# Performance work log

Measured on AMD Instinct MI355X. Metric: run time of the kernel, lower is better.

Reference implementation:

```python
import jax, jax.numpy as jnp
import numpy as np

NEG = -9e9  # large negative used by the original torch code for masking


def setup_inputs() -> dict:
    key = jax.random.key(0)
    k1, k2, k3, k4 = jax.random.split(key, 4)
    B, N, L, D = 64, 128, 64, 768
    return {
        "text_embeddings": jax.random.normal(k1, (B, N, D), dtype=jnp.float32),
        "image_embeddings": jax.random.normal(k2, (B, L, D), dtype=jnp.float32),
        "text_mask": jax.random.randint(k3, (B, N), 0, 2, dtype=jnp.int32),
        "image_mask": jax.random.randint(k4, (B, L), 0, 2, dtype=jnp.int32),
    }


def _grounding(text_emb, image_emb, text_mask, image_mask):
    # Vectorized version of the B x B python loop in score_grounding.
    tm = text_mask.astype(text_emb.dtype)   # [B, N]
    im = image_mask.astype(text_emb.dtype)  # [B, L]
    # pairwise mask: mask[i, j, n, l] = text_mask[i, n] * image_mask[j, l]
    mask = tm[:, None, :, None] * im[None, :, None, :]            # [B, B, N, L]
    att = jnp.einsum('ind,jld->ijnl', text_emb, image_emb) * mask  # [B, B, N, L]
    att = jnp.where(att * mask != 0, att, NEG)
    # softmax over image spans (last dim), masked
    aw_first = jax.nn.softmax(att, axis=-1) * mask
    score1 = (aw_first * att).sum(-1).mean(-1)                     # [B, B]
    # softmax over text spans (dim 2 == the N axis), masked (transpose trick in torch)
    aw_second = jax.nn.softmax(att, axis=2) * mask
    score2 = (aw_second * att).sum(-1).mean(-1)                    # [B, B]
    sent_scores = score1 + score2                                  # [B, B]
    B = text_emb.shape[0]
    idx = jnp.arange(B)
    token_scores = att[idx, idx]                                   # diagonal pairs, [B, N, L]
    return sent_scores, token_scores


def reference(text_embeddings, image_embeddings, text_mask, image_mask):
    B = text_embeddings.shape[0]
    S, token_scores = _grounding(text_embeddings, image_embeddings, text_mask, image_mask)
    # text_emb_i2s = softmax(att_weights) @ image_emb
    text_emb_i2s = jnp.einsum('bnl,bld->bnd', jax.nn.softmax(token_scores, axis=-1), image_embeddings)
    # loss = -(sum diag logsoftmax(S, dim=1) + sum diag logsoftmax(S.T, dim=1)) / n
    ls1 = jnp.diagonal(jax.nn.log_softmax(S, axis=1))
    ls2 = jnp.diagonal(jax.nn.log_softmax(S.T, axis=1))
    loss = -(jnp.sum(ls1) + jnp.sum(ls2)) / B
    return loss, text_emb_i2s
```

## Files before the change

### kernel.cpp

```cpp
#include <hip/hip_runtime.h>
#include <math.h>

#define BSZ 64
#define NN  128
#define LL  64
#define DD  768
#define NEGV (-9e9f)

#define TQ (BSZ * NN * DD / 4)
#define IQ (BSZ * LL * DD / 4)

typedef _Float16 f16x8 __attribute__((ext_vector_type(8)));
typedef __attribute__((ext_vector_type(4))) float f32x4;

__device__ __forceinline__ void gl_lds16(const void* g, void* l) {
    __builtin_amdgcn_global_load_lds(
        (const __attribute__((address_space(1))) void*)g,
        (__attribute__((address_space(3))) void*)l, 16, 0, 0);
}

__global__ __launch_bounds__(256) void k_prep(
    const float4* __restrict__ t4, const float4* __restrict__ g4,
    ushort4* __restrict__ A, ushort4* __restrict__ B)
{
    int id = blockIdx.x * 256 + threadIdx.x;
    const float4* src; ushort4* dst; int idx;
    if (id < TQ) { src = t4; dst = A; idx = id; }
    else         { src = g4; dst = B; idx = id - TQ; }
    float4 x = src[idx];
    _Float16 h0 = (_Float16)x.x, h1 = (_Float16)x.y;
    _Float16 h2 = (_Float16)x.z, h3 = (_Float16)x.w;
    ushort4 o;
    o.x = __builtin_bit_cast(unsigned short, h0);
    o.y = __builtin_bit_cast(unsigned short, h1);
    o.z = __builtin_bit_cast(unsigned short, h2);
    o.w = __builtin_bit_cast(unsigned short, h3);
    dst[idx] = o;
}

__device__ __forceinline__ void stage_chunk(
    const unsigned short* __restrict__ pa, const unsigned short* __restrict__ pb,
    int k0, char* buf, int wave, int lane)
{
    int rsub = lane >> 3;
    int k8s  = lane & 7;
#pragma unroll
    for (int c = 0; c < 4; c++) {
        int r  = c * 64 + wave * 8 + rsub;
        int k8 = k8s ^ (r & 7);
        gl_lds16(pa + (size_t)r * DD + k0 + k8 * 8, buf + c * 8192 + wave * 1024);
        gl_lds16(pb + (size_t)r * DD + k0 + k8 * 8, buf + 32768 + c * 8192 + wave * 1024);
    }
}

__global__ __launch_bounds__(512, 2) void k_scores(
    const unsigned short* __restrict__ A, const unsigned short* __restrict__ B,
    const int* __restrict__ tmask, const int* __restrict__ imask,
    float* __restrict__ S, float* __restrict__ W)
{
    __shared__ __align__(16) char stage[2][65536];
    __shared__ float tmi[256];
    __shared__ float imj[256];
    __shared__ float rowredL[256][4];
    __shared__ float cpmax[4][256];
    __shared__ float cpes[4][256];
    __shared__ float cpws[4][256];

    const int bid = blockIdx.x;
    const int grp = bid >> 4, idx = bid & 15;
    const int ip = (grp >> 2) * 4 + (idx >> 2);
    const int jq = (grp & 3) * 4 + (idx & 3);

    const int tid  = threadIdx.x;
    const int wave = tid >> 6;
    const int lane = tid & 63;
    const int quad = lane >> 4;
    const int l15  = lane & 15;
    const int wr   = wave & 3;
    const int wc   = wave >> 2;
    const int ih   = wr >> 1;

    if (tid < 256) tmi[tid] = tmask[ip * 256 + tid] ? 1.f : 0.f;
    else           imj[tid - 256] = imask[jq * 256 + (tid - 256)] ? 1.f : 0.f;

    const unsigned short* pa = A + (size_t)ip * 2 * NN * DD;
    const unsigned short* pb = B + (size_t)jq * 4 * LL * DD;

    f32x4 acc[4][8];
    const f32x4 zf = {0.f, 0.f, 0.f, 0.f};
#pragma unroll
    for (int tr = 0; tr < 4; tr++)
#pragma unroll
        for (int tc = 0; tc < 8; tc++) acc[tr][tc] = zf;

    stage_chunk(pa, pb, 0, stage[0], wave, lane);
    __syncthreads();

    for (int c = 0; c < 12; c++) {
        if (c + 1 < 12)
            stage_chunk(pa, pb, (c + 1) << 6, stage[(c + 1) & 1], wave, lane);
        const char* Ab = stage[c & 1];
        const char* Bb = Ab + 32768;
#pragma unroll
        for (int s = 0; s < 2; s++) {
            int sw = (((s * 4 + quad) ^ (l15 & 7)) << 4);
            f16x8 af[4], bfr[8];
#pragma unroll
            for (int tr = 0; tr < 4; tr++) {
                int row = wr * 64 + tr * 16 + l15;
                af[tr] = *(const f16x8*)(Ab + (row << 7) + sw);
            }
#pragma unroll
            for (int tc = 0; tc < 8; tc++) {
                int col = wc * 128 + tc * 16 + l15;
                bfr[tc] = *(const f16x8*)(Bb + (col << 7) + sw);
            }
#pragma unroll
            for (int tr = 0; tr < 4; tr++)
#pragma unroll
                for (int tc = 0; tc < 8; tc++)
                    acc[tr][tc] = __builtin_amdgcn_mfma_f32_16x16x32_f16(
                        af[tr], bfr[tc], acc[tr][tc], 0, 0, 0);
        }
        __syncthreads();
    }

    float tmr[4][4];
    float imc[8];
#pragma unroll
    for (int tr = 0; tr < 4; tr++)
#pragma unroll
        for (int rr = 0; rr < 4; rr++)
            tmr[tr][rr] = tmi[wr * 64 + tr * 16 + quad * 4 + rr];
#pragma unroll
    for (int tc = 0; tc < 8; tc++)
        imc[tc] = imj[wc * 128 + tc * 16 + l15];

    const bool isdiag = (jq == (ip >> 1));
    const int  jneed  = ip * 2 + ih - jq * 4;

#pragma unroll
    for (int tr = 0; tr < 4; tr++) {
#pragma unroll
        for (int rr = 0; rr < 4; rr++) {
            int row = wr * 64 + tr * 16 + quad * 4 + rr;
            float tm = tmr[tr][rr];
#pragma unroll
            for (int jl = 0; jl < 2; jl++) {
                float vmv[4];
                float m = -INFINITY;
#pragma unroll
                for (int t = 0; t < 4; t++) {
                    int tc = jl * 4 + t;
                    float v = acc[tr][tc][rr];
                    float vm = (tm != 0.f && imc[tc] != 0.f && v != 0.f) ? v : NEGV;
                    vmv[t] = vm;
                    m = fmaxf(m, vm);
                }
                m = fmaxf(m, __shfl_xor(m, 1));
                m = fmaxf(m, __shfl_xor(m, 2));
                m = fmaxf(m, __shfl_xor(m, 4));
                m = fmaxf(m, __shfl_xor(m, 8));
                float ss = 0.f, ws = 0.f;
#pragma unroll
                for (int t = 0; t < 4; t++) {
                    float e = __expf(vmv[t] - m);
                    ss += e;
                    ws += imc[jl * 4 + t] * e * vmv[t];
                }
                ss += __shfl_xor(ss, 1); ss += __shfl_xor(ss, 2);
                ss += __shfl_xor(ss, 4); ss += __shfl_xor(ss, 8);
                ws += __shfl_xor(ws, 1); ws += __shfl_xor(ws, 2);
                ws += __shfl_xor(ws, 4); ws += __shfl_xor(ws, 8);
                if (l15 == 0) rowredL[row][wc * 2 + jl] = tm * (ws / ss);
                if (isdiag && (wc * 2 + jl) == jneed) {
                    float inv = 1.f / ss;
                    float* Wb = W + (size_t)(ip * 2 + ih) * LL * NN;
                    int n = row & 127;
#pragma unroll
                    for (int t = 0; t < 4; t++) {
                        float e = __expf(vmv[t] - m) * inv;
                        Wb[(size_t)(t * 16 + l15) * NN + n] = e;
                    }
                }
            }
        }
    }

#pragma unroll
    for (int tc = 0; tc < 8; tc++) {
        int col = wc * 128 + tc * 16 + l15;
        float cm = -INFINITY;
#pragma unroll
        for (int tr = 0; tr < 4; tr++)
#pragma unroll
            for (int rr = 0; rr < 4; rr++) {
                float v = acc[tr][tc][rr];
                float vm = (tmr[tr][rr] != 0.f && imc[tc] != 0.f && v != 0.f) ? v : NEGV;
                cm = fmaxf(cm, vm);
            }
        cm = fmaxf(cm, __shfl_xor(cm, 16));
        cm = fmaxf(cm, __shfl_xor(cm, 32));
        if (quad == 0) cpmax[wr][col] = cm;
    }
    __syncthreads();

#pragma unroll
    for (int tc = 0; tc < 8; tc++) {
        int col = wc * 128 + tc * 16 + l15;
        float m2 = fmaxf(cpmax[ih * 2][col], cpmax[ih * 2 + 1][col]);
        float es = 0.f, ws = 0.f;
#pragma unroll
        for (int tr = 0; tr < 4; tr++)
#pragma unroll
            for (int rr = 0; rr < 4; rr++) {
                float v = acc[tr][tc][rr];
                float tm = tmr[tr][rr];
                float vm = (tm != 0.f && imc[tc] != 0.f && v != 0.f) ? v : NEGV;
                float e = __expf(vm - m2);
                es += e;
                ws += tm * e * vm;
            }
        es += __shfl_xor(es, 16); es += __shfl_xor(es, 32);
        ws += __shfl_xor(ws, 16); ws += __shfl_xor(ws, 32);
        if (quad == 0) { cpes[wr][col] = es; cpws[wr][col] = ws; }
    }
    __syncthreads();

    {
        int aih = wave >> 2, jloc = wave & 3;
        float p = rowredL[aih * 128 + lane][jloc]
                + rowredL[aih * 128 + 64 + lane][jloc];
        int col = jloc * 64 + lane;
        float es = cpes[aih * 2][col] + cpes[aih * 2 + 1][col];
        float ws = cpws[aih * 2][col] + cpws[aih * 2 + 1][col];
        p += imj[col] * (ws / es);
#pragma unroll
        for (int off = 32; off; off >>= 1) p += __shfl_down(p, off);
        if (lane == 0)
            S[(ip * 2 + aih) * BSZ + jq * 4 + jloc] = p * (1.f / 128.f);
    }
}

__global__ __launch_bounds__(256) void k_i2s(
    const float* __restrict__ W, const float* __restrict__ img,
    float* __restrict__ out)
{
    __shared__ float Ws[LL * NN];
    const int b = blockIdx.x, tid = threadIdx.x;
    const float* Wb = W + (size_t)b * LL * NN;
#pragma unroll
    for (int q = 0; q < 8; q++) {
        int o = (tid + q * 256) * 4;
        *(float4*)&Ws[o] = *(const float4*)&Wb[o];
    }
    __syncthreads();

    const int d = blockIdx.y * 256 + tid;
    const float* ib = img + (size_t)b * LL * DD + d;
    float* ob = out + 1 + (size_t)b * NN * DD + d;

    for (int ng = 0; ng < 8; ng++) {
        float acc[16];
#pragma unroll
        for (int q = 0; q < 16; q++) acc[q] = 0.f;
        for (int l = 0; l < LL; l++) {
            float g = ib[(size_t)l * DD];
            const float* wrow = &Ws[l * NN + ng * 16];
            float4 w0 = *(const float4*)(wrow);
            float4 w1 = *(const float4*)(wrow + 4);
            float4 w2 = *(const float4*)(wrow + 8);
            float4 w3 = *(const float4*)(wrow + 12);
            acc[0]  = fmaf(w0.x, g, acc[0]);  acc[1]  = fmaf(w0.y, g, acc[1]);
            acc[2]  = fmaf(w0.z, g, acc[2]);  acc[3]  = fmaf(w0.w, g, acc[3]);
            acc[4]  = fmaf(w1.x, g, acc[4]);  acc[5]  = fmaf(w1.y, g, acc[5]);
            acc[6]  = fmaf(w1.z, g, acc[6]);  acc[7]  = fmaf(w1.w, g, acc[7]);
            acc[8]  = fmaf(w2.x, g, acc[8]);  acc[9]  = fmaf(w2.y, g, acc[9]);
            acc[10] = fmaf(w2.z, g, acc[10]); acc[11] = fmaf(w2.w, g, acc[11]);
            acc[12] = fmaf(w3.x, g, acc[12]); acc[13] = fmaf(w3.y, g, acc[13]);
            acc[14] = fmaf(w3.z, g, acc[14]); acc[15] = fmaf(w3.w, g, acc[15]);
        }
#pragma unroll
        for (int q = 0; q < 16; q++)
            ob[(size_t)(ng * 16 + q) * DD] = acc[q];
    }
}

__global__ __launch_bounds__(256) void k_loss(
    const float* __restrict__ S, float* __restrict__ out)
{
    __shared__ float Ss[BSZ * BSZ];
    const int tid = threadIdx.x;
#pragma unroll
    for (int q = 0; q < 16; q++) Ss[tid + q * 256] = S[tid + q * 256];
    __syncthreads();
    if (tid < 64) {
        float diag = Ss[tid * BSZ + tid];
        float m1 = -INFINITY, m2 = -INFINITY;
        for (int jj = 0; jj < BSZ; jj++) {
            m1 = fmaxf(m1, Ss[tid * BSZ + jj]);
            m2 = fmaxf(m2, Ss[jj * BSZ + tid]);
        }
        float s1 = 0.f, s2 = 0.f;
        for (int jj = 0; jj < BSZ; jj++) {
            s1 += __expf(Ss[tid * BSZ + jj] - m1);
            s2 += __expf(Ss[jj * BSZ + tid] - m2);
        }
        float p = 2.f * diag - (m1 + logf(s1)) - (m2 + logf(s2));
#pragma unroll
        for (int off = 32; off; off >>= 1) p += __shfl_down(p, off);
        if (tid == 0) out[0] = -p / (float)BSZ;
    }
}

extern "C" void kernel_launch(void* const* d_in, const int* in_sizes, int n_in,
                              void* d_out, int out_size, void* d_ws, size_t ws_size,
                              hipStream_t stream)
{
    (void)in_sizes; (void)n_in; (void)out_size; (void)ws_size;
    const float* text = (const float*)d_in[0];
    const float* img  = (const float*)d_in[1];
    const int*   tm   = (const int*)d_in[2];
    const int*   im   = (const int*)d_in[3];
    float* out = (float*)d_out;

    char* ws = (char*)d_ws;
    unsigned short* A = (unsigned short*)(ws);
    unsigned short* B = (unsigned short*)(ws + 12582912);
    float* S = (float*)(ws + 18874368);
    float* W = (float*)(ws + 18890752);

    k_prep<<<(TQ + IQ) / 256, 256, 0, stream>>>(
        (const float4*)text, (const float4*)img, (ushort4*)A, (ushort4*)B);

    k_scores<<<512, 512, 0, stream>>>(A, B, tm, im, S, W);

    dim3 g2(BSZ, 3);
    k_i2s<<<g2, 256, 0, stream>>>(W, img, out);

    k_loss<<<1, 256, 0, stream>>>(S, out);
}
```

Measured before the change: 211.6 us.

## Shrink score-kernel tiles to 128x128 with 256 threads and K=32 stages

Each k_scores block now handles one text item against two image items (a 128x128 tile) instead of two text items against four image items (256x256), with 256 threads, a 32-wide K step and a new LDS swizzle. The launch grows from 512 to 2048 blocks and LDS use drops sharply, aiming for more blocks per CU and better load balance across the GPU. In exchange, each operand byte is reused less, so global/L2 traffic roughly doubles, and the K loop has twice as many barriers.

```diff
diff --git a/kernel.cpp b/kernel.cpp
--- a/kernel.cpp
+++ b/kernel.cpp
@@ -42,102 +42,96 @@
     const unsigned short* __restrict__ pa, const unsigned short* __restrict__ pb,
     int k0, char* buf, int wave, int lane)
 {
-    int rsub = lane >> 3;
-    int k8s  = lane & 7;
-#pragma unroll
-    for (int c = 0; c < 4; c++) {
-        int r  = c * 64 + wave * 8 + rsub;
-        int k8 = k8s ^ (r & 7);
-        gl_lds16(pa + (size_t)r * DD + k0 + k8 * 8, buf + c * 8192 + wave * 1024);
-        gl_lds16(pb + (size_t)r * DD + k0 + k8 * 8, buf + 32768 + c * 8192 + wave * 1024);
-    }
-}
-
-__global__ __launch_bounds__(512, 2) void k_scores(
+    int k8s = lane & 3;
+#pragma unroll
+    for (int c = 0; c < 2; c++) {
+        int r  = c * 64 + wave * 16 + (lane >> 2);
+        int k8 = k8s ^ ((r >> 1) & 3);
+        gl_lds16(pa + (size_t)r * DD + k0 + k8 * 8, buf + c * 4096 + wave * 1024);
+        gl_lds16(pb + (size_t)r * DD + k0 + k8 * 8, buf + 8192 + c * 4096 + wave * 1024);
+    }
+}
+
+__global__ __launch_bounds__(256, 3) void k_scores(
     const unsigned short* __restrict__ A, const unsigned short* __restrict__ B,
     const int* __restrict__ tmask, const int* __restrict__ imask,
     float* __restrict__ S, float* __restrict__ W)
 {
-    __shared__ __align__(16) char stage[2][65536];
-    __shared__ float tmi[256];
-    __shared__ float imj[256];
-    __shared__ float rowredL[256][4];
-    __shared__ float cpmax[4][256];
-    __shared__ float cpes[4][256];
-    __shared__ float cpws[4][256];
+    __shared__ __align__(16) char stage[2][16384];
+    __shared__ float tmi[NN];
+    __shared__ float imj[NN];
+    __shared__ float rowredL[NN][2];
+    __shared__ float cpmax[2][NN];
+    __shared__ float cpes[2][NN];
+    __shared__ float cpws[2][NN];
 
     const int bid = blockIdx.x;
     const int grp = bid >> 4, idx = bid & 15;
-    const int ip = (grp >> 2) * 4 + (idx >> 2);
-    const int jq = (grp & 3) * 4 + (idx & 3);
+    const int gi = grp >> 3, gj = grp & 7;
+    const int i  = gi * 4 + (idx >> 2);
+    const int jp = gj * 4 + (idx & 3);
+    const int j0 = jp * 2;
 
     const int tid  = threadIdx.x;
     const int wave = tid >> 6;
     const int lane = tid & 63;
     const int quad = lane >> 4;
     const int l15  = lane & 15;
-    const int wr   = wave & 3;
-    const int wc   = wave >> 2;
-    const int ih   = wr >> 1;
-
-    if (tid < 256) tmi[tid] = tmask[ip * 256 + tid] ? 1.f : 0.f;
-    else           imj[tid - 256] = imask[jq * 256 + (tid - 256)] ? 1.f : 0.f;
-
-    const unsigned short* pa = A + (size_t)ip * 2 * NN * DD;
-    const unsigned short* pb = B + (size_t)jq * 4 * LL * DD;
-
-    f32x4 acc[4][8];
+    const int wr   = wave & 1;
+    const int wc   = wave >> 1;
+
+    if (tid < NN) {
+        tmi[tid] = tmask[i * NN + tid] ? 1.f : 0.f;
+        imj[tid] = imask[j0 * LL + tid] ? 1.f : 0.f;
+    }
+
+    const unsigned short* pa = A + (size_t)i * NN * DD;
+    const unsigned short* pb = B + (size_t)j0 * LL * DD;
+
+    f32x4 acc[4][4];
     const f32x4 zf = {0.f, 0.f, 0.f, 0.f};
 #pragma unroll
     for (int tr = 0; tr < 4; tr++)
 #pragma unroll
-        for (int tc = 0; tc < 8; tc++) acc[tr][tc] = zf;
+        for (int tc = 0; tc < 4; tc++) acc[tr][tc] = zf;
 
     stage_chunk(pa, pb, 0, stage[0], wave, lane);
     __syncthreads();
 
-    for (int c = 0; c < 12; c++) {
-        if (c + 1 < 12)
-            stage_chunk(pa, pb, (c + 1) << 6, stage[(c + 1) & 1], wave, lane);
+    for (int c = 0; c < 24; c++) {
+        if (c + 1 < 24)
+            stage_chunk(pa, pb, (c + 1) << 5, stage[(c + 1) & 1], wave, lane);
         const char* Ab = stage[c & 1];
-        const char* Bb = Ab + 32768;
-#pragma unroll
-        for (int s = 0; s < 2; s++) {
-            int sw = (((s * 4 + quad) ^ (l15 & 7)) << 4);
-            f16x8 af[4], bfr[8];
-#pragma unroll
-            for (int tr = 0; tr < 4; tr++) {
-                int row = wr * 64 + tr * 16 + l15;
-                af[tr] = *(const f16x8*)(Ab + (row << 7) + sw);
-            }
-#pragma unroll
-            for (int tc = 0; tc < 8; tc++) {
-                int col = wc * 128 + tc * 16 + l15;
-                bfr[tc] = *(const f16x8*)(Bb + (col << 7) + sw);
-            }
-#pragma unroll
-            for (int tr = 0; tr < 4; tr++)
-#pragma unroll
-                for (int tc = 0; tc < 8; tc++)
-                    acc[tr][tc] = __builtin_amdgcn_mfma_f32_16x16x32_f16(
-                        af[tr], bfr[tc], acc[tr][tc], 0, 0, 0);
-        }
+        const char* Bb = Ab + 8192;
+        f16x8 af[4], bfr[4];
+#pragma unroll
+        for (int t = 0; t < 4; t++) {
+            int row = wr * 64 + t * 16 + l15;
+            af[t]  = *(const f16x8*)(Ab + ((row << 2) + (quad ^ ((row >> 1) & 3))) * 16);
+            int col = wc * 64 + t * 16 + l15;
+            bfr[t] = *(const f16x8*)(Bb + ((col << 2) + (quad ^ ((col >> 1) & 3))) * 16);
+        }
+#pragma unroll
+        for (int tr = 0; tr < 4; tr++)
+#pragma unroll
+            for (int tc = 0; tc < 4; tc++)
+                acc[tr][tc] = __builtin_amdgcn_mfma_f32_16x16x32_f16(
+                    af[tr], bfr[tc], acc[tr][tc], 0, 0, 0);
         __syncthreads();
     }
 
     float tmr[4][4];
-    float imc[8];
+    float imc[4];
 #pragma unroll
     for (int tr = 0; tr < 4; tr++)
 #pragma unroll
         for (int rr = 0; rr < 4; rr++)
             tmr[tr][rr] = tmi[wr * 64 + tr * 16 + quad * 4 + rr];
 #pragma unroll
-    for (int tc = 0; tc < 8; tc++)
-        imc[tc] = imj[wc * 128 + tc * 16 + l15];
-
-    const bool isdiag = (jq == (ip >> 1));
-    const int  jneed  = ip * 2 + ih - jq * 4;
+    for (int tc = 0; tc < 4; tc++)
+        imc[tc] = imj[wc * 64 + tc * 16 + l15];
+
+    const bool wdiag = (jp == (i >> 1)) && (wc == (i & 1));
 
 #pragma unroll
     for (int tr = 0; tr < 4; tr++) {
@@ -145,51 +139,44 @@
         for (int rr = 0; rr < 4; rr++) {
             int row = wr * 64 + tr * 16 + quad * 4 + rr;
             float tm = tmr[tr][rr];
-#pragma unroll
-            for (int jl = 0; jl < 2; jl++) {
-                float vmv[4];
-                float m = -INFINITY;
-#pragma unroll
-                for (int t = 0; t < 4; t++) {
-                    int tc = jl * 4 + t;
-                    float v = acc[tr][tc][rr];
-                    float vm = (tm != 0.f && imc[tc] != 0.f && v != 0.f) ? v : NEGV;
-                    vmv[t] = vm;
-                    m = fmaxf(m, vm);
-                }
-                m = fmaxf(m, __shfl_xor(m, 1));
-                m = fmaxf(m, __shfl_xor(m, 2));
-                m = fmaxf(m, __shfl_xor(m, 4));
-                m = fmaxf(m, __shfl_xor(m, 8));
-                float ss = 0.f, ws = 0.f;
-#pragma unroll
-                for (int t = 0; t < 4; t++) {
-                    float e = __expf(vmv[t] - m);
-                    ss += e;
-                    ws += imc[jl * 4 + t] * e * vmv[t];
-                }
-                ss += __shfl_xor(ss, 1); ss += __shfl_xor(ss, 2);
-                ss += __shfl_xor(ss, 4); ss += __shfl_xor(ss, 8);
-                ws += __shfl_xor(ws, 1); ws += __shfl_xor(ws, 2);
-                ws += __shfl_xor(ws, 4); ws += __shfl_xor(ws, 8);
-                if (l15 == 0) rowredL[row][wc * 2 + jl] = tm * (ws / ss);
-                if (isdiag && (wc * 2 + jl) == jneed) {
-                    float inv = 1.f / ss;
-                    float* Wb = W + (size_t)(ip * 2 + ih) * LL * NN;
-                    int n = row & 127;
-#pragma unroll
-                    for (int t = 0; t < 4; t++) {
-                        float e = __expf(vmv[t] - m) * inv;
-                        Wb[(size_t)(t * 16 + l15) * NN + n] = e;
-                    }
-                }
-            }
-        }
-    }
-
-#pragma unroll
-    for (int tc = 0; tc < 8; tc++) {
-        int col = wc * 128 + tc * 16 + l15;
+            float vmv[4];
+            float m = -INFINITY;
+#pragma unroll
+            for (int tc = 0; tc < 4; tc++) {
+                float v = acc[tr][tc][rr];
+                float vm = (tm != 0.f && imc[tc] != 0.f && v != 0.f) ? v : NEGV;
+                vmv[tc] = vm;
+                m = fmaxf(m, vm);
+            }
+            m = fmaxf(m, __shfl_xor(m, 1));
+            m = fmaxf(m, __shfl_xor(m, 2));
+            m = fmaxf(m, __shfl_xor(m, 4));
+            m = fmaxf(m, __shfl_xor(m, 8));
+            float ss = 0.f, ws = 0.f;
+#pragma unroll
+            for (int tc = 0; tc < 4; tc++) {
+                float e = __expf(vmv[tc] - m);
+                ss += e;
+                ws += imc[tc] * e * vmv[tc];
+            }
+            ss += __shfl_xor(ss, 1); ss += __shfl_xor(ss, 2);
+            ss += __shfl_xor(ss, 4); ss += __shfl_xor(ss, 8);
+            ws += __shfl_xor(ws, 1); ws += __shfl_xor(ws, 2);
+            ws += __shfl_xor(ws, 4); ws += __shfl_xor(ws, 8);
+            if (l15 == 0) rowredL[row][wc] = tm * (ws / ss);
+            if (wdiag) {
+                float inv = 1.f / ss;
+                float* Wb = W + (size_t)i * LL * NN;
+#pragma unroll
+                for (int tc = 0; tc < 4; tc++)
+                    Wb[(size_t)(tc * 16 + l15) * NN + row] = __expf(vmv[tc] - m) * inv;
+            }
+        }
+    }
+
+#pragma unroll
+    for (int tc = 0; tc < 4; tc++) {
+        int col = wc * 64 + tc * 16 + l15;
         float cm = -INFINITY;
 #pragma unroll
         for (int tr = 0; tr < 4; tr++)
@@ -206,9 +193,9 @@
     __syncthreads();
 
 #pragma unroll
-    for (int tc = 0; tc < 8; tc++) {
-        int col = wc * 128 + tc * 16 + l15;
-        float m2 = fmaxf(cpmax[ih * 2][col], cpmax[ih * 2 + 1][col]);
+    for (int tc = 0; tc < 4; tc++) {
+        int col = wc * 64 + tc * 16 + l15;
+        float m2 = fmaxf(cpmax[0][col], cpmax[1][col]);
         float es = 0.f, ws = 0.f;
 #pragma unroll
         for (int tr = 0; tr < 4; tr++)
@@ -227,18 +214,16 @@
     }
     __syncthreads();
 
-    {
-        int aih = wave >> 2, jloc = wave & 3;
-        float p = rowredL[aih * 128 + lane][jloc]
-                + rowredL[aih * 128 + 64 + lane][jloc];
-        int col = jloc * 64 + lane;
-        float es = cpes[aih * 2][col] + cpes[aih * 2 + 1][col];
-        float ws = cpws[aih * 2][col] + cpws[aih * 2 + 1][col];
+    if (wave < 2) {
+        int jl = wave;
+        float p = rowredL[lane][jl] + rowredL[64 + lane][jl];
+        int col = jl * 64 + lane;
+        float es = cpes[0][col] + cpes[1][col];
+        float ws = cpws[0][col] + cpws[1][col];
         p += imj[col] * (ws / es);
 #pragma unroll
         for (int off = 32; off; off >>= 1) p += __shfl_down(p, off);
-        if (lane == 0)
-            S[(ip * 2 + aih) * BSZ + jq * 4 + jloc] = p * (1.f / 128.f);
+        if (lane == 0) S[i * BSZ + j0 + jl] = p * (1.f / 128.f);
     }
 }
 
@@ -333,7 +318,7 @@
     k_prep<<<(TQ + IQ) / 256, 256, 0, stream>>>(
         (const float4*)text, (const float4*)img, (ushort4*)A, (ushort4*)B);
 
-    k_scores<<<512, 512, 0, stream>>>(A, B, tm, im, S, W);
+    k_scores<<<2048, 256, 0, stream>>>(A, B, tm, im, S, W);
 
     dim3 g2(BSZ, 3);
     k_i2s<<<g2, 256, 0, stream>>>(W, img, out);
```

Measured after the change: 210.3 us. Within noise of the previous version (-0.6%).
